# Optimization experiments

Hardware: AMD Instinct MI355X
Metric: run time of the kernel (lower is better)

## Reference

```python
import jax, jax.numpy as jnp
import numpy as np
from math import sqrt

N_HEADS = 16

def _rope(t, freqs):
    # t: [b, n, l, hd]; freqs: [l, hd//2, 2] (real, imag of unit rotations)
    b, n, l, hd = t.shape
    t2 = t.reshape(b, n, l, hd // 2, 2)
    tr, ti = t2[..., 0], t2[..., 1]
    fr, fi = freqs[..., 0], freqs[..., 1]  # broadcast over b, n
    out_r = tr * fr - ti * fi
    out_i = tr * fi + ti * fr
    return jnp.stack([out_r, out_i], axis=-1).reshape(b, n, l, hd)

def setup_inputs() -> dict:
    key = jax.random.key(0)
    ks = jax.random.split(key, 6)
    B, L, D = 2, 2048, 1024
    HD = D // N_HEADS
    x = jax.random.normal(ks[0], (B, L, D), dtype=jnp.float32)
    # proper rotary frequencies: theta_i = 10000^{-2i/hd}, angle = pos * theta
    inv = 1.0 / (10000.0 ** (np.arange(0, HD, 2, dtype=np.float32) / HD))  # [HD//2]
    ang = np.arange(L, dtype=np.float32)[:, None] * inv[None, :]           # [L, HD//2]
    freqs = jnp.asarray(np.stack([np.cos(ang), np.sin(ang)], axis=-1))     # [L, HD//2, 2]
    # additive causal mask
    causal = jnp.tril(jnp.ones((L, L), dtype=bool))
    attention_mask = jnp.where(causal, 0.0, -1e9).astype(jnp.float32)[None, None]
    init = 1.0 / sqrt(D)
    Wq = jax.random.normal(ks[1], (D, D), dtype=jnp.float32) * init
    Wk = jax.random.normal(ks[2], (D, D), dtype=jnp.float32) * init
    Wv = jax.random.normal(ks[3], (D, D), dtype=jnp.float32) * init
    Wo = jax.random.normal(ks[4], (D, D), dtype=jnp.float32) * init
    return {"x": x, "freqs": freqs, "attention_mask": attention_mask,
            "Wq": Wq, "Wk": Wk, "Wv": Wv, "Wo": Wo}

def reference(x, freqs, attention_mask, Wq, Wk, Wv, Wo):
    b, l, d = x.shape
    n = N_HEADS
    hd = d // n
    scale = sqrt(hd)

    def split_heads(t):  # [b, l, d] -> [b, n, l, hd]
        return t.reshape(b, l, n, hd).transpose(0, 2, 1, 3)

    q = split_heads(x @ Wq.T)
    k = split_heads(x @ Wk.T)
    v = split_heads(x @ Wv.T)
    q = _rope(q, freqs)
    k = _rope(k, freqs)
    scores = jnp.einsum('bnqd,bnkd->bnqk', q, k) / scale
    attn = jax.nn.softmax(scores + attention_mask, axis=-1)
    out = jnp.einsum('bnqk,bnkd->bnqd', attn, v)
    out = out.transpose(0, 2, 1, 3).reshape(b, l, d)
    return out @ Wo.T
```

## Files before the change

### kernel.cpp

```cpp
#include <hip/hip_runtime.h>
#include <stdint.h>

#define LSEQ 2048
#define DMODEL 1024
#define NHEADS 16
#define HDIM 64
#define MROWS 4096

typedef __attribute__((ext_vector_type(8))) short short8;
typedef __attribute__((ext_vector_type(4))) float f32x4;
typedef __attribute__((ext_vector_type(16))) float f32x16;

static __device__ __forceinline__ unsigned short f2bf(float f) {
    unsigned u = __builtin_bit_cast(unsigned, f);
    u += 0x7fffu + ((u >> 16) & 1u);
    return (unsigned short)(u >> 16);
}
static __device__ __forceinline__ unsigned packbf2(float a, float b) {
    return (unsigned)f2bf(a) | ((unsigned)f2bf(b) << 16);
}

static __device__ __forceinline__ void gl2lds16(const unsigned short* g, unsigned short* l) {
    __builtin_amdgcn_global_load_lds(
        (const __attribute__((address_space(1))) unsigned int*)g,
        (__attribute__((address_space(3))) unsigned int*)l, 16, 0, 0);
}

__global__ void cast_all(const float* __restrict__ x,  const float* __restrict__ Wq,
                         const float* __restrict__ Wk, const float* __restrict__ Wv,
                         const float* __restrict__ Wo,
                         unsigned short* __restrict__ xb,
                         unsigned short* __restrict__ wqkv,
                         unsigned short* __restrict__ wo) {
    int i = blockIdx.x * blockDim.x + threadIdx.x;
    const float4* src;
    ushort4* dst;
    if (i < 1048576) {
        src = (const float4*)x + i;
        dst = (ushort4*)xb + i;
    } else {
        int t = i - 1048576;
        int w = t >> 18;
        int j = t & 262143;
        const float* s = (w == 0) ? Wq : (w == 1) ? Wk : (w == 2) ? Wv : Wo;
        src = (const float4*)s + j;
        dst = (w == 3) ? ((ushort4*)wo + j) : ((ushort4*)wqkv + (size_t)w * 262144 + j);
    }
    float4 v = *src;
    ushort4 o;
    o.x = f2bf(v.x); o.y = f2bf(v.y); o.z = f2bf(v.z); o.w = f2bf(v.w);
    *dst = o;
}

template <int TM, bool OUT_BF16>
__global__ __launch_bounds__(256) void gemm_nt(const unsigned short* __restrict__ A,
                                               const unsigned short* __restrict__ Bw,
                                               void* __restrict__ C,
                                               int Kdim, int ldc) {
    constexpr int WM = TM / 2;
    __shared__ unsigned short As[TM * 32];
    __shared__ unsigned short Bs[128 * 32];
    int tid = threadIdx.x;
    int lane = tid & 63, wave = tid >> 6;
    int row16 = lane & 15, quad = lane >> 4;
    int wm = wave & 1, wn = wave >> 1;
    int m0 = blockIdx.x * TM;
    int n0 = blockIdx.y * 128;

    int srow = wave * 16 + (lane >> 2);
    int scol = (lane & 3) * 8;
    const unsigned short* Ag = A  + (size_t)(m0 + srow) * Kdim + scol;
    const unsigned short* Bg = Bw + (size_t)(n0 + srow) * Kdim + scol;
    unsigned short* Asw = As + wave * 512;
    unsigned short* Bsw = Bs + wave * 512;

    f32x4 acc[WM / 16][4];
    #pragma unroll
    for (int i = 0; i < WM / 16; ++i)
        #pragma unroll
        for (int j = 0; j < 4; ++j) acc[i][j] = (f32x4){0.f, 0.f, 0.f, 0.f};

    for (int k0 = 0; k0 < Kdim; k0 += 32) {
        #pragma unroll
        for (int i = 0; i < TM / 64; ++i)
            gl2lds16(Ag + (size_t)i * 64 * Kdim + k0, Asw + i * 2048);
        gl2lds16(Bg + k0, Bsw);
        gl2lds16(Bg + (size_t)64 * Kdim + k0, Bsw + 2048);
        __syncthreads();

        short8 af[WM / 16], bf_[4];
        #pragma unroll
        for (int mi = 0; mi < WM / 16; ++mi)
            af[mi] = *(const short8*)(As + (wm * WM + mi * 16 + row16) * 32 + quad * 8);
        #pragma unroll
        for (int ni = 0; ni < 4; ++ni)
            bf_[ni] = *(const short8*)(Bs + (wn * 64 + ni * 16 + row16) * 32 + quad * 8);
        #pragma unroll
        for (int mi = 0; mi < WM / 16; ++mi)
            #pragma unroll
            for (int ni = 0; ni < 4; ++ni)
                acc[mi][ni] = __builtin_amdgcn_mfma_f32_16x16x32_bf16(af[mi], bf_[ni], acc[mi][ni], 0, 0, 0);
        __syncthreads();
    }

    int orow = m0 + wm * WM + quad * 4;
    int ocol = n0 + wn * 64 + row16;
    #pragma unroll
    for (int mi = 0; mi < WM / 16; ++mi)
        #pragma unroll
        for (int ni = 0; ni < 4; ++ni)
            #pragma unroll
            for (int r = 0; r < 4; ++r) {
                size_t idx = (size_t)(orow + mi * 16 + r) * ldc + (ocol + ni * 16);
                if (OUT_BF16) ((unsigned short*)C)[idx] = f2bf(acc[mi][ni][r]);
                else          ((float*)C)[idx]          = acc[mi][ni][r];
            }
}

__global__ __launch_bounds__(256) void gemm_qkv(const unsigned short* __restrict__ A,
                                                const unsigned short* __restrict__ Bw,
                                                const float* __restrict__ freqs,
                                                unsigned short* __restrict__ qh,
                                                unsigned short* __restrict__ kh,
                                                unsigned short* __restrict__ vt) {
    const int Kdim = DMODEL;
    __shared__ unsigned short As[128 * 32];
    __shared__ unsigned short Bs[128 * 32];
    int tid = threadIdx.x;
    int lane = tid & 63, wave = tid >> 6;
    int row16 = lane & 15, quad = lane >> 4;
    int wm = wave & 1, wn = wave >> 1;
    int m0 = blockIdx.x * 128;
    int n0 = blockIdx.y * 128;

    int srow = wave * 16 + (lane >> 2);
    int scol = (lane & 3) * 8;
    const unsigned short* Ag  = A  + (size_t)(m0 + srow) * Kdim + scol;
    const unsigned short* Ag2 = Ag + (size_t)64 * Kdim;
    const unsigned short* Bg  = Bw + (size_t)(n0 + srow) * Kdim + scol;
    const unsigned short* Bg2 = Bg + (size_t)64 * Kdim;
    unsigned short* Asw = As + wave * 512;
    unsigned short* Bsw = Bs + wave * 512;

    f32x4 acc[4][4];
    #pragma unroll
    for (int i = 0; i < 4; ++i)
        #pragma unroll
        for (int j = 0; j < 4; ++j) acc[i][j] = (f32x4){0.f, 0.f, 0.f, 0.f};

    for (int k0 = 0; k0 < Kdim; k0 += 32) {
        gl2lds16(Ag  + k0, Asw);
        gl2lds16(Ag2 + k0, Asw + 2048);
        gl2lds16(Bg  + k0, Bsw);
        gl2lds16(Bg2 + k0, Bsw + 2048);
        __syncthreads();

        short8 af[4], bf_[4];
        #pragma unroll
        for (int mi = 0; mi < 4; ++mi)
            af[mi] = *(const short8*)(As + (wm * 64 + mi * 16 + row16) * 32 + quad * 8);
        #pragma unroll
        for (int ni = 0; ni < 4; ++ni)
            bf_[ni] = *(const short8*)(Bs + (wn * 64 + ni * 16 + row16) * 32 + quad * 8);
        #pragma unroll
        for (int mi = 0; mi < 4; ++mi)
            #pragma unroll
            for (int ni = 0; ni < 4; ++ni)
                acc[mi][ni] = __builtin_amdgcn_mfma_f32_16x16x32_bf16(af[mi], bf_[ni], acc[mi][ni], 0, 0, 0);
        __syncthreads();
    }

    int orow = m0 + wm * 64 + quad * 4;
    int ocol = n0 + wn * 64 + row16;
    int b = m0 >> 11;
    int region = n0 >> 10;

    if (region < 2) {
        unsigned short* dst = region ? kh : qh;
        int cbase = ocol - region * 1024;
        float sgn = (row16 & 1) ? 1.f : -1.f;
        #pragma unroll
        for (int ni = 0; ni < 4; ++ni) {
            int c = cbase + ni * 16;
            int head = c >> 6, d = c & 63, ii = d >> 1;
            unsigned short* hb = dst + (((size_t)(b * NHEADS + head)) * LSEQ) * HDIM + d;
            #pragma unroll
            for (int mi = 0; mi < 4; ++mi)
                #pragma unroll
                for (int r = 0; r < 4; ++r) {
                    int l = (orow + mi * 16 + r) & 2047;
                    float own = acc[mi][ni][r];
                    float par = __shfl_xor(own, 1);
                    float2 f = *(const float2*)(freqs + ((size_t)l * 32 + ii) * 2);
                    float out = own * f.x + par * (sgn * f.y);
                    hb[(size_t)l * HDIM] = f2bf(out);
                }
        }
    } else {
        #pragma unroll
        for (int ni = 0; ni < 4; ++ni) {
            int c = ocol - 2048 + ni * 16;
            int head = c >> 6, d = c & 63;
            size_t vbase = (((size_t)(b * NHEADS + head)) * HDIM + d) * LSEQ;
            #pragma unroll
            for (int mi = 0; mi < 4; ++mi) {
                int l0 = (orow + mi * 16) & 2047;
                ushort4 o;
                o.x = f2bf(acc[mi][ni][0]);
                o.y = f2bf(acc[mi][ni][1]);
                o.z = f2bf(acc[mi][ni][2]);
                o.w = f2bf(acc[mi][ni][3]);
                *(ushort4*)(vt + vbase + l0) = o;
            }
        }
    }
}

__global__ __launch_bounds__(256, 4) void attn_flash(const unsigned short* __restrict__ qh,
                                                     const unsigned short* __restrict__ kh,
                                                     const unsigned short* __restrict__ vt,
                                                     unsigned short* __restrict__ oh) {
    __shared__ char smem[16896];
    unsigned short* Kbuf = (unsigned short*)smem;
    unsigned short* Vbuf = (unsigned short*)(smem + 8192);
    float* mO = (float*)smem;
    float* mL = (float*)(smem + 16384);
    const float CS = 0.18033688011112042f;
    const float CB = 28.853900817779268f;

    int lane = threadIdx.x & 63;
    int wave = threadIdx.x >> 6;
    int l31 = lane & 31;
    int h   = lane >> 5;
    int kq  = wave >> 1, qq = wave & 1;

    int id  = blockIdx.x;
    int xcd = id & 7;
    int bn  = xcd * 4 + ((id >> 3) & 3);
    int s   = id >> 5;
    int u = s & 7, rnd = s >> 3;
    int qb = (rnd == 0) ? (31 - u) : (rnd == 1) ? (16 + u) : (rnd == 2) ? (15 - u) : u;
    int b = bn >> 4, n = bn & 15;

    const unsigned short* Qb = qh + (size_t)bn * LSEQ * HDIM;
    const unsigned short* Kb = kh + (size_t)bn * LSEQ * HDIM;
    const unsigned short* Vb = vt + (size_t)bn * HDIM * LSEQ;

    int q0 = qb * 64;
    int qabs = q0 + qq * 32 + l31;

    short8 qf[4];
    #pragma unroll
    for (int mf = 0; mf < 4; ++mf)
        qf[mf] = *(const short8*)(Qb + (size_t)(q0 + qq * 32 + l31) * HDIM + mf * 16 + h * 8);

    int sf  = wave >> 1;
    int m0s = (wave & 1) * 2;
    const unsigned short* kg = Kb + (size_t)(sf * 32 + l31) * HDIM + m0s * 16 + h * 8;
    const unsigned short* vg = Vb + (size_t)(sf * 32 + l31) * LSEQ + m0s * 16 + h * 8;
    unsigned short* kds = Kbuf + (sf * 4 + m0s) * 512;
    unsigned short* vds = Vbuf + (sf * 4 + m0s) * 512;

    f32x16 accO[2];
    #pragma unroll
    for (int i = 0; i < 16; ++i) { accO[0][i] = 0.f; accO[1][i] = 0.f; }
    float l_s = 0.f;

    int nk = qb + 1;
    for (int kt = 0; kt < nk; ++kt) {
        const unsigned short* kgk = kg + (size_t)kt * 64 * HDIM;
        const unsigned short* vgk = vg + kt * 64;
        gl2lds16(kgk, kds);       gl2lds16(kgk + 16, kds + 512);
        gl2lds16(vgk, vds);       gl2lds16(vgk + 16, vds + 512);
        __syncthreads();

        bool edge = (kt == nk - 1);
        bool dead = edge && (kq == 1) && (qq == 0);

        if (!dead) {
            f32x16 z;
            #pragma unroll
            for (int i = 0; i < 16; ++i) z[i] = 0.f;
            #pragma unroll
            for (int m = 0; m < 4; ++m) {
                short8 kf = *(const short8*)(Kbuf + (kq * 4 + m) * 512 + lane * 8);
                z = __builtin_amdgcn_mfma_f32_32x32x16_bf16(kf, qf[m], z, 0, 0, 0);
            }

            float p[16];
            bool maskz = edge && (kq == qq);
            #pragma unroll
            for (int r = 0; r < 16; ++r) {
                float e = __builtin_amdgcn_exp2f(z[r] * CS - CB);
                if (maskz) {
                    int kabs = kt * 64 + kq * 32 + (r & 3) + 8 * (r >> 2) + 4 * h;
                    if (kabs > qabs) e = 0.f;
                }
                p[r] = e;
            }
            float ps = 0.f;
            #pragma unroll
            for (int r = 0; r < 16; ++r) ps += p[r];
            l_s += ps;

            uint2 P4[4];
            #pragma unroll
            for (int g = 0; g < 4; ++g) {
                P4[g].x = packbf2(p[4 * g], p[4 * g + 1]);
                P4[g].y = packbf2(p[4 * g + 2], p[4 * g + 3]);
            }
            short8 bfr[2];
            bool hb = (h != 0);
            #pragma unroll
            for (int m = 0; m < 2; ++m) {
                uint2 own = hb ? P4[1 + 2 * m] : P4[2 * m];
                uint2 snd = hb ? P4[2 * m]     : P4[1 + 2 * m];
                uint2 rcv;
                rcv.x = __shfl_xor(snd.x, 32);
                rcv.y = __shfl_xor(snd.y, 32);
                uint4 bb;
                bb.x = hb ? rcv.x : own.x;
                bb.y = hb ? rcv.y : own.y;
                bb.z = hb ? own.x : rcv.x;
                bb.w = hb ? own.y : rcv.y;
                bfr[m] = __builtin_bit_cast(short8, bb);
            }

            #pragma unroll
            for (int dq = 0; dq < 2; ++dq)
                #pragma unroll
                for (int m = 0; m < 2; ++m) {
                    short8 vf = *(const short8*)(Vbuf + (dq * 4 + kq * 2 + m) * 512 + lane * 8);
                    accO[dq] = __builtin_amdgcn_mfma_f32_32x32x16_bf16(vf, bfr[m], accO[dq], 0, 0, 0);
                }
        }
        __syncthreads();
    }

    l_s += __shfl_xor(l_s, 32);

    if (kq == 1) {
        #pragma unroll
        for (int dq = 0; dq < 2; ++dq)
            #pragma unroll
            for (int r = 0; r < 16; ++r)
                mO[(qq * 2 + dq) * 1024 + r * 64 + lane] = accO[dq][r];
        mL[qq * 64 + lane] = l_s;
    }
    __syncthreads();
    if (kq == 0) {
        float inv = 1.0f / (l_s + mL[qq * 64 + lane]);
        #pragma unroll
        for (int dq = 0; dq < 2; ++dq)
            #pragma unroll
            for (int g = 0; g < 4; ++g) {
                float o0 = (accO[dq][4 * g]     + mO[(qq * 2 + dq) * 1024 + (4 * g)     * 64 + lane]) * inv;
                float o1 = (accO[dq][4 * g + 1] + mO[(qq * 2 + dq) * 1024 + (4 * g + 1) * 64 + lane]) * inv;
                float o2 = (accO[dq][4 * g + 2] + mO[(qq * 2 + dq) * 1024 + (4 * g + 2) * 64 + lane]) * inv;
                float o3 = (accO[dq][4 * g + 3] + mO[(qq * 2 + dq) * 1024 + (4 * g + 3) * 64 + lane]) * inv;
                ushort4 o;
                o.x = f2bf(o0); o.y = f2bf(o1); o.z = f2bf(o2); o.w = f2bf(o3);
                int d = dq * 32 + 8 * g + 4 * h;
                *(ushort4*)(oh + (size_t)(b * LSEQ + q0 + qq * 32 + l31) * DMODEL + n * HDIM + d) = o;
            }
    }
}

extern "C" void kernel_launch(void* const* d_in, const int* in_sizes, int n_in,
                              void* d_out, int out_size, void* d_ws, size_t ws_size,
                              hipStream_t stream) {
    const float* x     = (const float*)d_in[0];
    const float* freqs = (const float*)d_in[1];
    const float* Wq = (const float*)d_in[3];
    const float* Wk = (const float*)d_in[4];
    const float* Wv = (const float*)d_in[5];
    const float* Wo = (const float*)d_in[6];

    char* ws = (char*)d_ws;
    unsigned short* xb   = (unsigned short*)ws; ws += (size_t)MROWS * DMODEL * 2;
    unsigned short* wqkv = (unsigned short*)ws; ws += (size_t)3 * DMODEL * DMODEL * 2;
    unsigned short* wo   = (unsigned short*)ws; ws += (size_t)DMODEL * DMODEL * 2;
    unsigned short* qh   = (unsigned short*)ws; ws += (size_t)32 * LSEQ * HDIM * 2;
    unsigned short* kh   = (unsigned short*)ws; ws += (size_t)32 * LSEQ * HDIM * 2;
    unsigned short* vt   = (unsigned short*)ws; ws += (size_t)32 * HDIM * LSEQ * 2;
    unsigned short* oh   = (unsigned short*)ws; ws += (size_t)MROWS * DMODEL * 2;

    cast_all<<<8192, 256, 0, stream>>>(x, Wq, Wk, Wv, Wo, xb, wqkv, wo);

    gemm_qkv<<<dim3(MROWS / 128, 3072 / 128), 256, 0, stream>>>(xb, wqkv, freqs, qh, kh, vt);

    attn_flash<<<1024, 256, 0, stream>>>(qh, kh, vt, oh);

    gemm_nt<64, false><<<dim3(MROWS / 64, DMODEL / 128), 256, 0, stream>>>(oh, wo, (float*)d_out, DMODEL, DMODEL);
}
```

Baseline: 212.3 us.

## Restructure QKV GEMM into 256x256 tiles with 4-stage async LDS pipeline

```diff
diff --git a/kernel.cpp b/kernel.cpp
--- a/kernel.cpp
+++ b/kernel.cpp
@@ -117,79 +117,120 @@
             }
 }
 
-__global__ __launch_bounds__(256) void gemm_qkv(const unsigned short* __restrict__ A,
-                                                const unsigned short* __restrict__ Bw,
-                                                const float* __restrict__ freqs,
-                                                unsigned short* __restrict__ qh,
-                                                unsigned short* __restrict__ kh,
-                                                unsigned short* __restrict__ vt) {
-    const int Kdim = DMODEL;
-    __shared__ unsigned short As[128 * 32];
-    __shared__ unsigned short Bs[128 * 32];
-    int tid = threadIdx.x;
+#define QKV_PHASE(VN, T, DO_STAGE)                                          \
+  {                                                                         \
+    asm volatile("s_waitcnt vmcnt(" #VN ")" ::: "memory");                  \
+    __builtin_amdgcn_s_barrier();                                           \
+    __builtin_amdgcn_sched_barrier(0);                                      \
+    if (DO_STAGE) {                                                         \
+      int t3 = (T) + 3;                                                     \
+      int ws = (t3 & 3) * 16384;                                            \
+      const unsigned short* asrc = AgL + t3 * 32;                           \
+      const unsigned short* bsrc = BgL + t3 * 32;                           \
+      gl2lds16(asrc,                        lds + ws + stA);                \
+      gl2lds16(asrc + (size_t)128 * DMODEL, lds + ws + stA + 4096);         \
+      gl2lds16(bsrc,                        lds + ws + stB);                \
+      gl2lds16(bsrc + (size_t)128 * DMODEL, lds + ws + stB + 4096);         \
+    }                                                                       \
+    {                                                                       \
+      int rs = ((T) & 3) * 16384;                                           \
+      const unsigned short* Ar = lds + rs + rdA;                            \
+      const unsigned short* Br = lds + rs + 8192 + rdB;                     \
+      short8 bfr[4];                                                        \
+      _Pragma("unroll")                                                     \
+      for (int j = 0; j < 4; ++j) bfr[j] = *(const short8*)(Br + j * 512);  \
+      _Pragma("unroll")                                                     \
+      for (int q = 0; q < 2; ++q) {                                         \
+        short8 af[4];                                                       \
+        _Pragma("unroll")                                                   \
+        for (int i = 0; i < 4; ++i)                                         \
+          af[i] = *(const short8*)(Ar + q * 2048 + i * 512);                \
+        __builtin_amdgcn_s_setprio(1);                                      \
+        _Pragma("unroll")                                                   \
+        for (int i = 0; i < 4; ++i)                                         \
+          _Pragma("unroll")                                                 \
+          for (int j = 0; j < 4; ++j)                                       \
+            acc[q * 4 + i][j] = __builtin_amdgcn_mfma_f32_16x16x32_bf16(    \
+                af[i], bfr[j], acc[q * 4 + i][j], 0, 0, 0);                 \
+        __builtin_amdgcn_s_setprio(0);                                      \
+      }                                                                     \
+    }                                                                       \
+  }
+
+__global__ __launch_bounds__(512, 2) void gemm_qkv(const unsigned short* __restrict__ A,
+                                                   const unsigned short* __restrict__ Bw,
+                                                   const float* __restrict__ freqs,
+                                                   unsigned short* __restrict__ qh,
+                                                   unsigned short* __restrict__ kh,
+                                                   unsigned short* __restrict__ vt) {
+    extern __shared__ unsigned short lds[];
+
+    int tid  = threadIdx.x;
     int lane = tid & 63, wave = tid >> 6;
     int row16 = lane & 15, quad = lane >> 4;
     int wm = wave & 1, wn = wave >> 1;
-    int m0 = blockIdx.x * 128;
-    int n0 = blockIdx.y * 128;
-
-    int srow = wave * 16 + (lane >> 2);
-    int scol = (lane & 3) * 8;
-    const unsigned short* Ag  = A  + (size_t)(m0 + srow) * Kdim + scol;
-    const unsigned short* Ag2 = Ag + (size_t)64 * Kdim;
-    const unsigned short* Bg  = Bw + (size_t)(n0 + srow) * Kdim + scol;
-    const unsigned short* Bg2 = Bg + (size_t)64 * Kdim;
-    unsigned short* Asw = As + wave * 512;
-    unsigned short* Bsw = Bs + wave * 512;
-
-    f32x4 acc[4][4];
-    #pragma unroll
-    for (int i = 0; i < 4; ++i)
+
+    int id  = blockIdx.x;
+    int gid = (id & 7) * 24 + (id >> 3);
+    int bx = gid / 12, by = gid % 12;
+    int m0 = bx * 256, n0 = by * 256;
+
+    int off0 = tid * 16;
+    int g = off0 ^ (((off0 >> 7) & 3) << 4);
+    int srow = g >> 6;
+    int scol = (g & 63) >> 1;
+    const unsigned short* AgL = A  + (size_t)(m0 + srow) * DMODEL + scol;
+    const unsigned short* BgL = Bw + (size_t)(n0 + srow) * DMODEL + scol;
+
+    int stA = wave * 512;
+    int stB = 8192 + wave * 512;
+
+    int sw  = ((row16 >> 1) & 3) << 4;
+    int rdA = ((((wm * 128 + row16) * 64) + quad * 16) ^ sw) >> 1;
+    int rdB = ((((wn *  64 + row16) * 64) + quad * 16) ^ sw) >> 1;
+
+    f32x4 acc[8][4];
+    #pragma unroll
+    for (int i = 0; i < 8; ++i)
         #pragma unroll
         for (int j = 0; j < 4; ++j) acc[i][j] = (f32x4){0.f, 0.f, 0.f, 0.f};
 
-    for (int k0 = 0; k0 < Kdim; k0 += 32) {
-        gl2lds16(Ag  + k0, Asw);
-        gl2lds16(Ag2 + k0, Asw + 2048);
-        gl2lds16(Bg  + k0, Bsw);
-        gl2lds16(Bg2 + k0, Bsw + 2048);
-        __syncthreads();
-
-        short8 af[4], bf_[4];
-        #pragma unroll
-        for (int mi = 0; mi < 4; ++mi)
-            af[mi] = *(const short8*)(As + (wm * 64 + mi * 16 + row16) * 32 + quad * 8);
-        #pragma unroll
-        for (int ni = 0; ni < 4; ++ni)
-            bf_[ni] = *(const short8*)(Bs + (wn * 64 + ni * 16 + row16) * 32 + quad * 8);
-        #pragma unroll
-        for (int mi = 0; mi < 4; ++mi)
-            #pragma unroll
-            for (int ni = 0; ni < 4; ++ni)
-                acc[mi][ni] = __builtin_amdgcn_mfma_f32_16x16x32_bf16(af[mi], bf_[ni], acc[mi][ni], 0, 0, 0);
-        __syncthreads();
-    }
-
-    int orow = m0 + wm * 64 + quad * 4;
-    int ocol = n0 + wn * 64 + row16;
+    #pragma unroll
+    for (int p = 0; p < 3; ++p) {
+        int ws = p * 16384;
+        const unsigned short* asrc = AgL + p * 32;
+        const unsigned short* bsrc = BgL + p * 32;
+        gl2lds16(asrc,                        lds + ws + stA);
+        gl2lds16(asrc + (size_t)128 * DMODEL, lds + ws + stA + 4096);
+        gl2lds16(bsrc,                        lds + ws + stB);
+        gl2lds16(bsrc + (size_t)128 * DMODEL, lds + ws + stB + 4096);
+    }
+
+    for (int t = 0; t < 30; ++t) {
+        QKV_PHASE(8, t, (t < 29))
+    }
+    QKV_PHASE(4, 30, false)
+    QKV_PHASE(0, 31, false)
+
+    int region = n0 >> 10;
     int b = m0 >> 11;
-    int region = n0 >> 10;
+    int orow0 = m0 + wm * 128 + quad * 4;
+    int ocol0 = n0 + wn * 64 + row16;
 
     if (region < 2) {
         unsigned short* dst = region ? kh : qh;
-        int cbase = ocol - region * 1024;
         float sgn = (row16 & 1) ? 1.f : -1.f;
         #pragma unroll
-        for (int ni = 0; ni < 4; ++ni) {
-            int c = cbase + ni * 16;
+        for (int nf = 0; nf < 4; ++nf) {
+            int c = ocol0 - region * 1024 + nf * 16;
             int head = c >> 6, d = c & 63, ii = d >> 1;
-            unsigned short* hb = dst + (((size_t)(b * NHEADS + head)) * LSEQ) * HDIM + d;
-            #pragma unroll
-            for (int mi = 0; mi < 4; ++mi)
+            unsigned short* hb = dst + ((size_t)(b * NHEADS + head) * LSEQ) * HDIM + d;
+            #pragma unroll
+            for (int mf = 0; mf < 8; ++mf)
                 #pragma unroll
                 for (int r = 0; r < 4; ++r) {
-                    int l = (orow + mi * 16 + r) & 2047;
-                    float own = acc[mi][ni][r];
+                    int l = (orow0 + mf * 16 + r) & 2047;
+                    float own = acc[mf][nf][r];
                     float par = __shfl_xor(own, 1);
                     float2 f = *(const float2*)(freqs + ((size_t)l * 32 + ii) * 2);
                     float out = own * f.x + par * (sgn * f.y);
@@ -198,18 +239,18 @@
         }
     } else {
         #pragma unroll
-        for (int ni = 0; ni < 4; ++ni) {
-            int c = ocol - 2048 + ni * 16;
+        for (int nf = 0; nf < 4; ++nf) {
+            int c = ocol0 - 2048 + nf * 16;
             int head = c >> 6, d = c & 63;
-            size_t vbase = (((size_t)(b * NHEADS + head)) * HDIM + d) * LSEQ;
-            #pragma unroll
-            for (int mi = 0; mi < 4; ++mi) {
-                int l0 = (orow + mi * 16) & 2047;
+            size_t vbase = ((size_t)(b * NHEADS + head) * HDIM + d) * LSEQ;
+            #pragma unroll
+            for (int mf = 0; mf < 8; ++mf) {
+                int l0 = (orow0 + mf * 16) & 2047;
                 ushort4 o;
-                o.x = f2bf(acc[mi][ni][0]);
-                o.y = f2bf(acc[mi][ni][1]);
-                o.z = f2bf(acc[mi][ni][2]);
-                o.w = f2bf(acc[mi][ni][3]);
+                o.x = f2bf(acc[mf][nf][0]);
+                o.y = f2bf(acc[mf][nf][1]);
+                o.z = f2bf(acc[mf][nf][2]);
+                o.w = f2bf(acc[mf][nf][3]);
                 *(ushort4*)(vt + vbase + l0) = o;
             }
         }
@@ -385,9 +426,16 @@
     unsigned short* vt   = (unsigned short*)ws; ws += (size_t)32 * HDIM * LSEQ * 2;
     unsigned short* oh   = (unsigned short*)ws; ws += (size_t)MROWS * DMODEL * 2;
 
+    static bool attr_set = false;
+    if (!attr_set) {
+        (void)hipFuncSetAttribute((const void*)gemm_qkv,
+                                  hipFuncAttributeMaxDynamicSharedMemorySize, 131072);
+        attr_set = true;
+    }
+
     cast_all<<<8192, 256, 0, stream>>>(x, Wq, Wk, Wv, Wo, xb, wqkv, wo);
 
-    gemm_qkv<<<dim3(MROWS / 128, 3072 / 128), 256, 0, stream>>>(xb, wqkv, freqs, qh, kh, vt);
+    gemm_qkv<<<192, 512, 131072, stream>>>(xb, wqkv, freqs, qh, kh, vt);
 
     attn_flash<<<1024, 256, 0, stream>>>(qh, kh, vt, oh);
 
```

Result: faster. 205.4 us (-3.3%).
